# Kernel optimization log

Measured on AMD Instinct MI355X. Metric: run time of the kernel, lower is better.

## Reference

```python
import jax, jax.numpy as jnp
import numpy as np

N_HEAD = 16
LN_EPS = 1e-5


def setup_inputs() -> dict:
    key = jax.random.key(0)
    ks = jax.random.split(key, 12)
    B, S, D = 4, 1024, 1024
    s = 1.0 / np.sqrt(D)
    return {
        "Q": jax.random.normal(ks[0], (B, S, D), jnp.float32),
        "K": jax.random.normal(ks[1], (B, S, D), jnp.float32),
        "V": jax.random.normal(ks[2], (B, S, D), jnp.float32),
        # Linear weights stored torch-style [out, in]
        "Wq": jax.random.normal(ks[3], (D, D), jnp.float32) * s,
        "bq": jnp.zeros((D,), jnp.float32),
        "Wk": jax.random.normal(ks[4], (D, D), jnp.float32) * s,
        "bk": jnp.zeros((D,), jnp.float32),
        "Wv": jax.random.normal(ks[5], (D, D), jnp.float32) * s,
        "bv": jnp.zeros((D,), jnp.float32),
        "Wo": jax.random.normal(ks[6], (D, D), jnp.float32) * s,
        "bo": jnp.zeros((D,), jnp.float32),
        "ln_g": jnp.ones((D,), jnp.float32),
        "ln_b": jnp.zeros((D,), jnp.float32),
    }


def _layer_norm(x, g, b):
    mu = jnp.mean(x, axis=-1, keepdims=True)
    var = jnp.mean(jnp.square(x - mu), axis=-1, keepdims=True)
    return (x - mu) * jax.lax.rsqrt(var + LN_EPS) * g + b


def reference(Q, K, V, Wq, bq, Wk, bk, Wv, bv, Wo, bo, ln_g, ln_b):
    B, S, D = Q.shape
    H = N_HEAD
    dk = D // H
    # projections, split heads: [B, H, S, dk]
    q = (Q @ Wq.T + bq).reshape(B, S, H, dk).transpose(0, 2, 1, 3)
    k = (K @ Wk.T + bk).reshape(B, S, H, dk).transpose(0, 2, 1, 3)
    v = (V @ Wv.T + bv).reshape(B, S, H, dk).transpose(0, 2, 1, 3)
    scores = jnp.einsum("bhqd,bhkd->bhqk", q, k) / np.sqrt(dk)
    # NOTE: original module applies softmax twice (F.softmax then nn.Softmax)
    attn = jax.nn.softmax(jax.nn.softmax(scores, axis=-1), axis=-1)
    ctx = jnp.einsum("bhqk,bhkd->bhqd", attn, v)  # [B, H, S, dk]
    ctx = ctx.transpose(0, 2, 1, 3).reshape(B, S, D)
    out = ctx @ Wo.T + bo
    return _layer_norm(out + Q, ln_g, ln_b)
```

## Files before the change

### kernel.cpp

```cpp
#include <hip/hip_runtime.h>
#include <cstdint>
#include <cstddef>


typedef unsigned short ushort_t;
typedef __attribute__((ext_vector_type(8))) short bf16x8;
typedef __attribute__((ext_vector_type(8))) unsigned short us8;
typedef __attribute__((ext_vector_type(4))) unsigned short us4;
typedef __attribute__((ext_vector_type(4))) float f32x4;

#define MFMA16(a, b, c) __builtin_amdgcn_mfma_f32_16x16x32_bf16((a), (b), (c), 0, 0, 0)
#define EXP2F(x) __builtin_amdgcn_exp2f(x)
#define LOG2E 1.4426950408889634f

__device__ __forceinline__ float b2f(ushort_t u) {
  union { unsigned int i; float f; } x; x.i = ((unsigned int)u) << 16; return x.f;
}
__device__ __forceinline__ ushort_t f2b(float f) {
  union { unsigned int i; float f; } x; x.f = f;
  unsigned int r = (x.i + 0x7FFFu + ((x.i >> 16) & 1u)) >> 16;
  return (ushort_t)r;
}
__device__ __forceinline__ unsigned int cvtpk(float lo, float hi) {
  unsigned int r;
  asm("v_cvt_pk_bf16_f32 %0, %1, %2" : "=v"(r) : "v"(lo), "v"(hi));
  return r;
}
__device__ __forceinline__ us8 cvt8pk(float4 a, float4 b) {
  union { unsigned int u[4]; us8 v; } r;
  r.u[0] = cvtpk(a.x, a.y); r.u[1] = cvtpk(a.z, a.w);
  r.u[2] = cvtpk(b.x, b.y); r.u[3] = cvtpk(b.z, b.w);
  return r.v;
}

__device__ __forceinline__ void gll16(const ushort_t* g, ushort_t* l) {
  __builtin_amdgcn_global_load_lds(
      (const __attribute__((address_space(1))) void*)g,
      (__attribute__((address_space(3))) void*)l, 16, 0, 0);
}

__global__ __launch_bounds__(256, 8) void cvt4_kernel(
    const float* __restrict__ w0, const float* __restrict__ w1,
    const float* __restrict__ w2, const float* __restrict__ w3,
    ushort_t* __restrict__ dst) {
  const int which = blockIdx.y;
  const float* src = (which == 0) ? w0 : (which == 1) ? w1 : (which == 2) ? w2 : w3;
  const int i = (blockIdx.x * 256 + threadIdx.x) * 8;
  const float4 a = *(const float4*)(src + i);
  const float4 b = *(const float4*)(src + i + 4);
  *(us8*)(dst + (size_t)which * 1048576 + i) = cvt8pk(a, b);
}

__global__ __launch_bounds__(256, 3) void qkv_proj_kernel(
    const float* __restrict__ Qin, const float* __restrict__ Kin,
    const float* __restrict__ Vin,
    const ushort_t* __restrict__ wq, const ushort_t* __restrict__ wk,
    const ushort_t* __restrict__ wv,
    const float* __restrict__ bq, const float* __restrict__ bk,
    const float* __restrict__ bv,
    ushort_t* __restrict__ qb, ushort_t* __restrict__ kb,
    ushort_t* __restrict__ vb) {
  __shared__ __align__(16) ushort_t Asl0[128 * 32];
  __shared__ __align__(16) ushort_t Asl1[128 * 32];
  __shared__ __align__(16) ushort_t Bsl0[128 * 32];
  __shared__ __align__(16) ushort_t Bsl1[128 * 32];
  const float* A; const ushort_t* W; const float* bias; float scale;
  if (blockIdx.z == 0)      { A = Qin; W = wq; bias = bq; scale = 0.125f * LOG2E; }
  else if (blockIdx.z == 1) { A = Kin; W = wk; bias = bk; scale = 1.0f; }
  else                      { A = Vin; W = wv; bias = bv; scale = 1.0f; }
  const int l = blockIdx.x;
  const int xcd = l & 7, ii = l >> 3;
  const int m0 = (xcd * 4 + (ii >> 3)) * 128;
  const int n0 = (ii & 7) * 128;
  const int tid = threadIdx.x;
  const int wave = tid >> 6, lane = tid & 63;
  const int l15 = lane & 15, quad = lane >> 4;
  const int wr = wave >> 1, wc = wave & 1;

  const int ra = tid >> 2, ca = (tid & 3) * 8;
  const float* Ap0 = A + (size_t)(m0 + ra) * 1024 + ca;
  const float* Ap1 = A + (size_t)(m0 + ra + 64) * 1024 + ca;

  const ushort_t* Bg0 = W + (size_t)(n0 + wave * 32 + (lane >> 2)) * 1024 + (lane & 3) * 8;
  const ushort_t* Bg1 = W + (size_t)(n0 + wave * 32 + 16 + (lane >> 2)) * 1024 + (lane & 3) * 8;

  float4 xa0 = *(const float4*)(Ap0), xa1 = *(const float4*)(Ap0 + 4);
  float4 xa2 = *(const float4*)(Ap1), xa3 = *(const float4*)(Ap1 + 4);
  gll16(Bg0, Bsl0 + wave * 1024);
  gll16(Bg1, Bsl0 + wave * 1024 + 512);
  *(us8*)(Asl0 + ra * 32 + ca) = cvt8pk(xa0, xa1);
  *(us8*)(Asl0 + (ra + 64) * 32 + ca) = cvt8pk(xa2, xa3);
  float4 ya0 = *(const float4*)(Ap0 + 32), ya1 = *(const float4*)(Ap0 + 36);
  float4 ya2 = *(const float4*)(Ap1 + 32), ya3 = *(const float4*)(Ap1 + 36);
  asm volatile("s_waitcnt vmcnt(4) lgkmcnt(0)" ::: "memory");
  __builtin_amdgcn_s_barrier();

  f32x4 acc[4][4] = {};
#define QKV_COMPUTE(ASL, BSL)                                                   \
  {                                                                             \
    bf16x8 af[4], bfr[4];                                                       \
    _Pragma("unroll") for (int s = 0; s < 4; ++s)                               \
        af[s] = *(const bf16x8*)((ASL) + (wr * 64 + s * 16 + l15) * 32 + quad * 8); \
    _Pragma("unroll") for (int s = 0; s < 4; ++s)                               \
        bfr[s] = *(const bf16x8*)((BSL) + (wc * 64 + s * 16 + l15) * 32 + quad * 8); \
    _Pragma("unroll") for (int ms = 0; ms < 4; ++ms)                            \
        _Pragma("unroll") for (int ns = 0; ns < 4; ++ns)                        \
            acc[ms][ns] = MFMA16(af[ms], bfr[ns], acc[ms][ns]);                 \
  }

  for (int k0 = 0; k0 < 1024; k0 += 64) {
    {
      gll16(Bg0 + k0 + 32, Bsl1 + wave * 1024);
      gll16(Bg1 + k0 + 32, Bsl1 + wave * 1024 + 512);
      *(us8*)(Asl1 + ra * 32 + ca) = cvt8pk(ya0, ya1);
      *(us8*)(Asl1 + (ra + 64) * 32 + ca) = cvt8pk(ya2, ya3);
    }
    if (k0 + 64 < 1024) {
      xa0 = *(const float4*)(Ap0 + k0 + 64); xa1 = *(const float4*)(Ap0 + k0 + 68);
      xa2 = *(const float4*)(Ap1 + k0 + 64); xa3 = *(const float4*)(Ap1 + k0 + 68);
    }
    QKV_COMPUTE(Asl0, Bsl0)
    if (k0 + 64 < 1024) asm volatile("s_waitcnt vmcnt(4) lgkmcnt(0)" ::: "memory");
    else                asm volatile("s_waitcnt vmcnt(0) lgkmcnt(0)" ::: "memory");
    __builtin_amdgcn_s_barrier();
    if (k0 + 64 < 1024) {
      gll16(Bg0 + k0 + 64, Bsl0 + wave * 1024);
      gll16(Bg1 + k0 + 64, Bsl0 + wave * 1024 + 512);
      *(us8*)(Asl0 + ra * 32 + ca) = cvt8pk(xa0, xa1);
      *(us8*)(Asl0 + (ra + 64) * 32 + ca) = cvt8pk(xa2, xa3);
      if (k0 + 96 < 1024) {
        ya0 = *(const float4*)(Ap0 + k0 + 96); ya1 = *(const float4*)(Ap0 + k0 + 100);
        ya2 = *(const float4*)(Ap1 + k0 + 96); ya3 = *(const float4*)(Ap1 + k0 + 100);
      }
    }
    QKV_COMPUTE(Asl1, Bsl1)
    if (k0 + 96 < 1024)      asm volatile("s_waitcnt vmcnt(4) lgkmcnt(0)" ::: "memory");
    else                     asm volatile("s_waitcnt vmcnt(0) lgkmcnt(0)" ::: "memory");
    __builtin_amdgcn_s_barrier();
  }
#undef QKV_COMPUTE

  if (blockIdx.z != 2) {
    ushort_t* outp = (blockIdx.z == 0) ? qb : kb;
#pragma unroll
    for (int ns = 0; ns < 4; ++ns) {
      const int col = n0 + wc * 64 + ns * 16 + l15;
      const float bv_ = bias[col];
#pragma unroll
      for (int ms = 0; ms < 4; ++ms) {
        const int rowb = m0 + wr * 64 + ms * 16 + quad * 4;
#pragma unroll
        for (int r = 0; r < 4; ++r) {
          outp[(size_t)(rowb + r) * 1024 + col] =
              f2b((acc[ms][ns][r] + bv_) * scale);
        }
      }
    }
  } else {
#pragma unroll
    for (int ns = 0; ns < 4; ++ns) {
      const int col = n0 + wc * 64 + ns * 16 + l15;
      const float bv_ = bias[col];
      const int h = col >> 6, d = col & 63;
#pragma unroll
      for (int ms = 0; ms < 4; ++ms) {
        const int i0 = m0 + wr * 64 + ms * 16 + quad * 4;
        const int b = i0 >> 10, s0 = i0 & 1023;
        us4 pack;
#pragma unroll
        for (int r = 0; r < 4; ++r) pack[r] = f2b(acc[ms][ns][r] + bv_);
        *(us4*)(vb + ((size_t)(b * 16 + h) * 64 + d) * 1024 + s0) = pack;
      }
    }
  }
}

__global__ __launch_bounds__(256, 4) void attn_kernel(
    const ushort_t* __restrict__ qb, const ushort_t* __restrict__ kb,
    const ushort_t* __restrict__ vb, ushort_t* __restrict__ ctx) {
  __shared__ __align__(16) ushort_t Sh0[64 * 72];
  __shared__ __align__(16) ushort_t Sh1[64 * 72];
  __shared__ __align__(16) ushort_t Sh2[64 * 72];
  __shared__ __align__(16) ushort_t Sh3[64 * 72];

  const int tid = threadIdx.x, wave = tid >> 6, lane = tid & 63;
  const int l15 = lane & 15, quad = lane >> 4;
  const int l = blockIdx.x;
  const int xcd = l & 7, ii = l >> 3;
  const int bh = xcd * 8 + (ii >> 4);
  const int q0 = (ii & 15) * 64;
  const int b = bh >> 4, h = bh & 15;
  const ushort_t* qg = qb + ((size_t)b << 20) + h * 64;
  const ushort_t* kg = kb + ((size_t)b << 20) + h * 64;
  const ushort_t* vg = vb + ((size_t)bh << 16);

  const int kr0 = tid >> 3, kc0 = (tid & 7) * 8;
  const int kr1 = (tid + 256) >> 3, kc1 = kc0;
  const int o0 = kr0 * 72 + kc0, o1 = kr1 * 72 + kc1;

  *(us8*)(Sh0 + o0) = *(const us8*)(qg + (size_t)(q0 + kr0) * 1024 + kc0);
  *(us8*)(Sh0 + o1) = *(const us8*)(qg + (size_t)(q0 + kr1) * 1024 + kc1);
  us8 rk0 = *(const us8*)(kg + (size_t)kr0 * 1024 + kc0);
  us8 rk1 = *(const us8*)(kg + (size_t)kr1 * 1024 + kc1);
  *(us8*)(Sh1 + o0) = rk0;
  *(us8*)(Sh1 + o1) = rk1;
  rk0 = *(const us8*)(kg + (size_t)(64 + kr0) * 1024 + kc0);
  rk1 = *(const us8*)(kg + (size_t)(64 + kr1) * 1024 + kc1);
  __syncthreads();
  bf16x8 aqh[2];
  aqh[0] = *(const bf16x8*)(Sh0 + (wave * 16 + l15) * 72 + quad * 8);
  aqh[1] = *(const bf16x8*)(Sh0 + (wave * 16 + l15) * 72 + 32 + quad * 8);

  float z1 = 0.f;
  for (int kt = 0; kt < 16; ++kt) {
    const ushort_t* kcur = (kt & 1) ? Sh2 : Sh1;
    f32x4 sc[4] = {};
#pragma unroll
    for (int kk = 0; kk < 2; ++kk) {
#pragma unroll
      for (int ns = 0; ns < 4; ++ns) {
        const bf16x8 kf = *(const bf16x8*)(kcur + (ns * 16 + l15) * 72 + kk * 32 + quad * 8);
        sc[ns] = MFMA16(kf, aqh[kk], sc[ns]);
      }
    }
    if (kt < 15) {
      ushort_t* knxt = (kt & 1) ? Sh1 : Sh2;
      *(us8*)(knxt + o0) = rk0;
      *(us8*)(knxt + o1) = rk1;
      if (kt < 14) {
        rk0 = *(const us8*)(kg + (size_t)((kt + 2) * 64 + kr0) * 1024 + kc0);
        rk1 = *(const us8*)(kg + (size_t)((kt + 2) * 64 + kr1) * 1024 + kc1);
      }
    }
#pragma unroll
    for (int ns = 0; ns < 4; ++ns)
#pragma unroll
      for (int r = 0; r < 4; ++r) z1 += EXP2F(sc[ns][r]);
    asm volatile("s_waitcnt lgkmcnt(0)" ::: "memory");
    __builtin_amdgcn_s_barrier();
  }
  z1 += __shfl_xor(z1, 16, 64);
  z1 += __shfl_xor(z1, 32, 64);
  const float iz1 = LOG2E / z1;

  const int adr0 = ((((quad & 1) << 1) * 16) + l15) << 2;
  const int adr1 = adr0 + 64;

  f32x4 oac[4] = {};
  float z2 = 0.f;
  rk0 = *(const us8*)(kg + (size_t)kr0 * 1024 + kc0);
  rk1 = *(const us8*)(kg + (size_t)kr1 * 1024 + kc1);
  us8 rv0 = *(const us8*)(vg + (size_t)kr0 * 1024 + kc0);
  us8 rv1 = *(const us8*)(vg + (size_t)kr1 * 1024 + kc1);
  *(us8*)(Sh0 + o0) = rk0;
  *(us8*)(Sh0 + o1) = rk1;
  *(us8*)(Sh2 + o0) = rv0;
  *(us8*)(Sh2 + o1) = rv1;
  rk0 = *(const us8*)(kg + (size_t)(64 + kr0) * 1024 + kc0);
  rk1 = *(const us8*)(kg + (size_t)(64 + kr1) * 1024 + kc1);
  rv0 = *(const us8*)(vg + (size_t)kr0 * 1024 + 64 + kc0);
  rv1 = *(const us8*)(vg + (size_t)kr1 * 1024 + 64 + kc1);
  asm volatile("s_waitcnt lgkmcnt(0)" ::: "memory");
  __builtin_amdgcn_s_barrier();

  for (int kt = 0; kt < 16; ++kt) {
    const ushort_t* kcur = (kt & 1) ? Sh1 : Sh0;
    const ushort_t* vcur = (kt & 1) ? Sh3 : Sh2;
    f32x4 sc[4] = {};
#pragma unroll
    for (int kk = 0; kk < 2; ++kk) {
#pragma unroll
      for (int ns = 0; ns < 4; ++ns) {
        const bf16x8 kf = *(const bf16x8*)(kcur + (ns * 16 + l15) * 72 + kk * 32 + quad * 8);
        sc[ns] = MFMA16(kf, aqh[kk], sc[ns]);
      }
    }
    if (kt < 15) {
      ushort_t* knxt = (kt & 1) ? Sh0 : Sh1;
      ushort_t* vnxt = (kt & 1) ? Sh2 : Sh3;
      *(us8*)(knxt + o0) = rk0;
      *(us8*)(knxt + o1) = rk1;
      *(us8*)(vnxt + o0) = rv0;
      *(us8*)(vnxt + o1) = rv1;
      if (kt < 14) {
        rk0 = *(const us8*)(kg + (size_t)((kt + 2) * 64 + kr0) * 1024 + kc0);
        rk1 = *(const us8*)(kg + (size_t)((kt + 2) * 64 + kr1) * 1024 + kc1);
        rv0 = *(const us8*)(vg + (size_t)kr0 * 1024 + (kt + 2) * 64 + kc0);
        rv1 = *(const us8*)(vg + (size_t)kr1 * 1024 + (kt + 2) * 64 + kc1);
      }
    }
    unsigned int D[4][2];
#pragma unroll
    for (int ns = 0; ns < 4; ++ns) {
      const float e0 = EXP2F(EXP2F(sc[ns][0]) * iz1);
      const float e1 = EXP2F(EXP2F(sc[ns][1]) * iz1);
      const float e2 = EXP2F(EXP2F(sc[ns][2]) * iz1);
      const float e3 = EXP2F(EXP2F(sc[ns][3]) * iz1);
      z2 += (e0 + e1) + (e2 + e3);
      D[ns][0] = cvtpk(e0, e1);
      D[ns][1] = cvtpk(e2, e3);
    }
#pragma unroll
    for (int kk = 0; kk < 2; ++kk) {
      union { unsigned int u[4]; bf16x8 v; } pf;
#pragma unroll
      for (int t = 0; t < 4; ++t) {
        const int adr = (t >> 1) ? adr1 : adr0;
        const int lo = __builtin_amdgcn_ds_bpermute(adr, (int)D[2 * kk][t & 1]);
        const int hi = __builtin_amdgcn_ds_bpermute(adr, (int)D[2 * kk + 1][t & 1]);
        pf.u[t] = (unsigned int)((quad >= 2) ? hi : lo);
      }
#pragma unroll
      for (int ns2 = 0; ns2 < 4; ++ns2) {
        const bf16x8 vf = *(const bf16x8*)(vcur + (ns2 * 16 + l15) * 72 + kk * 32 + quad * 8);
        oac[ns2] = MFMA16(vf, pf.v, oac[ns2]);
      }
    }
    asm volatile("s_waitcnt lgkmcnt(0)" ::: "memory");
    __builtin_amdgcn_s_barrier();
  }

  z2 += __shfl_xor(z2, 16, 64);
  z2 += __shfl_xor(z2, 32, 64);
  const int s = q0 + wave * 16 + l15;
  ushort_t* crow = ctx + ((size_t)(b * 1024 + s)) * 1024 + h * 64;
#pragma unroll
  for (int ns2 = 0; ns2 < 4; ++ns2) {
    us4 pack;
#pragma unroll
    for (int r = 0; r < 4; ++r) pack[r] = f2b(oac[ns2][r] / z2);
    *(us4*)(crow + ns2 * 16 + quad * 4) = pack;
  }
}

__global__ __launch_bounds__(256, 4) void out_proj_kernel(
    const ushort_t* __restrict__ ctxp, const ushort_t* __restrict__ wo,
    const float* __restrict__ bo, ushort_t* __restrict__ pre) {
  __shared__ __align__(16) ushort_t Asl0[64 * 32];
  __shared__ __align__(16) ushort_t Asl1[64 * 32];
  __shared__ __align__(16) ushort_t Bsl0[128 * 32];
  __shared__ __align__(16) ushort_t Bsl1[128 * 32];
  const int tid = threadIdx.x;
  const int wave = tid >> 6, lane = tid & 63;
  const int l15 = lane & 15, quad = lane >> 4;
  const int wr = wave >> 1, wc = wave & 1;
  const int l = blockIdx.x;
  const int xcd = l & 7, ii = l >> 3;
  const int m0 = (xcd * 8 + (ii >> 3)) * 64;
  const int n0 = (ii & 7) * 128;

  const ushort_t* Ag = ctxp + (size_t)(m0 + wave * 16 + (lane >> 2)) * 1024 + (lane & 3) * 8;
  const ushort_t* Bg0 = wo + (size_t)(n0 + wave * 32 + (lane >> 2)) * 1024 + (lane & 3) * 8;
  const ushort_t* Bg1 = wo + (size_t)(n0 + wave * 32 + 16 + (lane >> 2)) * 1024 + (lane & 3) * 8;

  gll16(Ag, Asl0 + wave * 512);
  gll16(Bg0, Bsl0 + wave * 1024);
  gll16(Bg1, Bsl0 + wave * 1024 + 512);
  __syncthreads();

  f32x4 acc[2][4] = {};
#define OUTP_COMPUTE(ASL, BSL)                                                  \
  {                                                                             \
    bf16x8 af[2], bfr[4];                                                       \
    _Pragma("unroll") for (int s = 0; s < 2; ++s)                               \
        af[s] = *(const bf16x8*)((ASL) + (wr * 32 + s * 16 + l15) * 32 + quad * 8); \
    _Pragma("unroll") for (int s = 0; s < 4; ++s)                               \
        bfr[s] = *(const bf16x8*)((BSL) + (wc * 64 + s * 16 + l15) * 32 + quad * 8); \
    _Pragma("unroll") for (int ms = 0; ms < 2; ++ms)                            \
        _Pragma("unroll") for (int ns = 0; ns < 4; ++ns)                        \
            acc[ms][ns] = MFMA16(af[ms], bfr[ns], acc[ms][ns]);                 \
  }

  for (int k0 = 0; k0 < 1024; k0 += 64) {
    {
      gll16(Ag + k0 + 32, Asl1 + wave * 512);
      gll16(Bg0 + k0 + 32, Bsl1 + wave * 1024);
      gll16(Bg1 + k0 + 32, Bsl1 + wave * 1024 + 512);
    }
    OUTP_COMPUTE(Asl0, Bsl0)
    __syncthreads();
    if (k0 + 64 < 1024) {
      gll16(Ag + k0 + 64, Asl0 + wave * 512);
      gll16(Bg0 + k0 + 64, Bsl0 + wave * 1024);
      gll16(Bg1 + k0 + 64, Bsl0 + wave * 1024 + 512);
    }
    OUTP_COMPUTE(Asl1, Bsl1)
    __syncthreads();
  }
#undef OUTP_COMPUTE

#pragma unroll
  for (int ns = 0; ns < 4; ++ns) {
    const int col = n0 + wc * 64 + ns * 16 + l15;
    const float bv_ = bo[col];
#pragma unroll
    for (int ms = 0; ms < 2; ++ms) {
      const int rowb = m0 + wr * 32 + ms * 16 + quad * 4;
#pragma unroll
      for (int r = 0; r < 4; ++r) {
        pre[(size_t)(rowb + r) * 1024 + col] = f2b(acc[ms][ns][r] + bv_);
      }
    }
  }
}

__global__ __launch_bounds__(256, 4) void ln_kernel(
    const ushort_t* __restrict__ pre, const float* __restrict__ Q,
    const float* __restrict__ g, const float* __restrict__ bta,
    float* __restrict__ out) {
  const int row = blockIdx.x;
  const int tid = threadIdx.x;
  const size_t base = (size_t)row * 1024 + tid * 4;
  const ushort4 p4 = *(const ushort4*)(pre + base);
  const float4 q4 = *(const float4*)(Q + base);
  float v[4] = {b2f(p4.x) + q4.x, b2f(p4.y) + q4.y,
                b2f(p4.z) + q4.z, b2f(p4.w) + q4.w};
  float s1 = v[0] + v[1] + v[2] + v[3];
  float s2 = v[0]*v[0] + v[1]*v[1] + v[2]*v[2] + v[3]*v[3];
#pragma unroll
  for (int off = 1; off < 64; off <<= 1) {
    s1 += __shfl_xor(s1, off, 64);
    s2 += __shfl_xor(s2, off, 64);
  }
  __shared__ float r1[4], r2[4];
  const int wave = tid >> 6, lane = tid & 63;
  if (lane == 0) { r1[wave] = s1; r2[wave] = s2; }
  __syncthreads();
  const float t1 = r1[0] + r1[1] + r1[2] + r1[3];
  const float t2 = r2[0] + r2[1] + r2[2] + r2[3];
  const float mu = t1 * (1.0f / 1024.0f);
  const float var = t2 * (1.0f / 1024.0f) - mu * mu;
  const float inv = rsqrtf(var + 1e-5f);
  const int c0 = tid * 4;
#pragma unroll
  for (int j = 0; j < 4; ++j) {
    const int c = c0 + j;
    out[(size_t)row * 1024 + c] = (v[j] - mu) * inv * g[c] + bta[c];
  }
}

extern "C" void kernel_launch(void* const* d_in, const int* in_sizes, int n_in,
                              void* d_out, int out_size, void* d_ws, size_t ws_size,
                              hipStream_t stream) {
  const float* Q  = (const float*)d_in[0];
  const float* K  = (const float*)d_in[1];
  const float* V  = (const float*)d_in[2];
  const float* Wq = (const float*)d_in[3];
  const float* bq = (const float*)d_in[4];
  const float* Wk = (const float*)d_in[5];
  const float* bk = (const float*)d_in[6];
  const float* Wv = (const float*)d_in[7];
  const float* bv = (const float*)d_in[8];
  const float* Wo = (const float*)d_in[9];
  const float* bo = (const float*)d_in[10];
  const float* lg = (const float*)d_in[11];
  const float* lb = (const float*)d_in[12];

  char* ws = (char*)d_ws;
  ushort_t* qb  = (ushort_t*)(ws);
  ushort_t* kb  = (ushort_t*)(ws + ((size_t)8  << 20));
  ushort_t* vb  = (ushort_t*)(ws + ((size_t)16 << 20));
  ushort_t* pre = (ushort_t*)(ws);

  ushort_t* dptr  = (ushort_t*)d_out;
  ushort_t* wo_bf = dptr;
  ushort_t* wq_bf = dptr + 1048576;
  ushort_t* wk_bf = dptr + 2097152;
  ushort_t* wv_bf = dptr + 3145728;
  ushort_t* ctx   = dptr + 4194304;
  float*    out   = (float*)d_out;

  cvt4_kernel<<<dim3(512, 4), 256, 0, stream>>>(Wo, Wq, Wk, Wv, dptr);
  qkv_proj_kernel<<<dim3(256, 1, 3), 256, 0, stream>>>(Q, K, V, wq_bf, wk_bf, wv_bf,
                                                       bq, bk, bv, qb, kb, vb);
  attn_kernel<<<dim3(1024), 256, 0, stream>>>(qb, kb, vb, ctx);
  out_proj_kernel<<<dim3(512), 256, 0, stream>>>(ctx, wo_bf, bo, pre);
  ln_kernel<<<dim3(4096), 256, 0, stream>>>(pre, Q, lg, lb, out);
}
```

Before: 235.4 us.

## Triple-buffer weight tiles in QKV and output projection GEMMs

Both projection GEMMs move from double-buffered to triple-buffered LDS for the async global-to-LDS weight (and ctx) loads. Each load is now issued two k-steps ahead, and the waitcnt counts are relaxed so each barrier waits only for the oldest tile. The aim is to hide more global memory latency behind the MFMA work. In exchange it uses more LDS per block, which may reduce occupancy, and it adds pointer rotation plus peeled epilogue steps.

```diff
diff --git a/kernel.cpp b/kernel.cpp
--- a/kernel.cpp
+++ b/kernel.cpp
@@ -62,8 +62,7 @@
     ushort_t* __restrict__ vb) {
   __shared__ __align__(16) ushort_t Asl0[128 * 32];
   __shared__ __align__(16) ushort_t Asl1[128 * 32];
-  __shared__ __align__(16) ushort_t Bsl0[128 * 32];
-  __shared__ __align__(16) ushort_t Bsl1[128 * 32];
+  __shared__ __align__(16) ushort_t Bsl[3][128 * 32];
   const float* A; const ushort_t* W; const float* bias; float scale;
   if (blockIdx.z == 0)      { A = Qin; W = wq; bias = bq; scale = 0.125f * LOG2E; }
   else if (blockIdx.z == 1) { A = Kin; W = wk; bias = bk; scale = 1.0f; }
@@ -83,16 +82,21 @@
 
   const ushort_t* Bg0 = W + (size_t)(n0 + wave * 32 + (lane >> 2)) * 1024 + (lane & 3) * 8;
   const ushort_t* Bg1 = W + (size_t)(n0 + wave * 32 + 16 + (lane >> 2)) * 1024 + (lane & 3) * 8;
+  ushort_t* Ba = Bsl[0];
+  ushort_t* Bb = Bsl[1];
+  ushort_t* Bc = Bsl[2];
 
   float4 xa0 = *(const float4*)(Ap0), xa1 = *(const float4*)(Ap0 + 4);
   float4 xa2 = *(const float4*)(Ap1), xa3 = *(const float4*)(Ap1 + 4);
-  gll16(Bg0, Bsl0 + wave * 1024);
-  gll16(Bg1, Bsl0 + wave * 1024 + 512);
+  gll16(Bg0, Ba + wave * 1024);
+  gll16(Bg1, Ba + wave * 1024 + 512);
+  gll16(Bg0 + 32, Bb + wave * 1024);
+  gll16(Bg1 + 32, Bb + wave * 1024 + 512);
+  float4 ya0 = *(const float4*)(Ap0 + 32), ya1 = *(const float4*)(Ap0 + 36);
+  float4 ya2 = *(const float4*)(Ap1 + 32), ya3 = *(const float4*)(Ap1 + 36);
   *(us8*)(Asl0 + ra * 32 + ca) = cvt8pk(xa0, xa1);
   *(us8*)(Asl0 + (ra + 64) * 32 + ca) = cvt8pk(xa2, xa3);
-  float4 ya0 = *(const float4*)(Ap0 + 32), ya1 = *(const float4*)(Ap0 + 36);
-  float4 ya2 = *(const float4*)(Ap1 + 32), ya3 = *(const float4*)(Ap1 + 36);
-  asm volatile("s_waitcnt vmcnt(4) lgkmcnt(0)" ::: "memory");
+  asm volatile("s_waitcnt vmcnt(6) lgkmcnt(0)" ::: "memory");
   __builtin_amdgcn_s_barrier();
 
   f32x4 acc[4][4] = {};
@@ -108,36 +112,34 @@
             acc[ms][ns] = MFMA16(af[ms], bfr[ns], acc[ms][ns]);                 \
   }
 
-  for (int k0 = 0; k0 < 1024; k0 += 64) {
-    {
-      gll16(Bg0 + k0 + 32, Bsl1 + wave * 1024);
-      gll16(Bg1 + k0 + 32, Bsl1 + wave * 1024 + 512);
-      *(us8*)(Asl1 + ra * 32 + ca) = cvt8pk(ya0, ya1);
-      *(us8*)(Asl1 + (ra + 64) * 32 + ca) = cvt8pk(ya2, ya3);
-    }
-    if (k0 + 64 < 1024) {
-      xa0 = *(const float4*)(Ap0 + k0 + 64); xa1 = *(const float4*)(Ap0 + k0 + 68);
-      xa2 = *(const float4*)(Ap1 + k0 + 64); xa3 = *(const float4*)(Ap1 + k0 + 68);
-    }
-    QKV_COMPUTE(Asl0, Bsl0)
-    if (k0 + 64 < 1024) asm volatile("s_waitcnt vmcnt(4) lgkmcnt(0)" ::: "memory");
-    else                asm volatile("s_waitcnt vmcnt(0) lgkmcnt(0)" ::: "memory");
+  for (int i = 0; i < 15; ++i) {
+    const int k0 = i * 64;
+    gll16(Bg0 + k0 + 64, Bc + wave * 1024);
+    gll16(Bg1 + k0 + 64, Bc + wave * 1024 + 512);
+    xa0 = *(const float4*)(Ap0 + k0 + 64); xa1 = *(const float4*)(Ap0 + k0 + 68);
+    xa2 = *(const float4*)(Ap1 + k0 + 64); xa3 = *(const float4*)(Ap1 + k0 + 68);
+    QKV_COMPUTE(Asl0, Ba)
+    *(us8*)(Asl1 + ra * 32 + ca) = cvt8pk(ya0, ya1);
+    *(us8*)(Asl1 + (ra + 64) * 32 + ca) = cvt8pk(ya2, ya3);
+    asm volatile("s_waitcnt vmcnt(6) lgkmcnt(0)" ::: "memory");
     __builtin_amdgcn_s_barrier();
-    if (k0 + 64 < 1024) {
-      gll16(Bg0 + k0 + 64, Bsl0 + wave * 1024);
-      gll16(Bg1 + k0 + 64, Bsl0 + wave * 1024 + 512);
-      *(us8*)(Asl0 + ra * 32 + ca) = cvt8pk(xa0, xa1);
-      *(us8*)(Asl0 + (ra + 64) * 32 + ca) = cvt8pk(xa2, xa3);
-      if (k0 + 96 < 1024) {
-        ya0 = *(const float4*)(Ap0 + k0 + 96); ya1 = *(const float4*)(Ap0 + k0 + 100);
-        ya2 = *(const float4*)(Ap1 + k0 + 96); ya3 = *(const float4*)(Ap1 + k0 + 100);
-      }
-    }
-    QKV_COMPUTE(Asl1, Bsl1)
-    if (k0 + 96 < 1024)      asm volatile("s_waitcnt vmcnt(4) lgkmcnt(0)" ::: "memory");
-    else                     asm volatile("s_waitcnt vmcnt(0) lgkmcnt(0)" ::: "memory");
+    gll16(Bg0 + k0 + 96, Ba + wave * 1024);
+    gll16(Bg1 + k0 + 96, Ba + wave * 1024 + 512);
+    ya0 = *(const float4*)(Ap0 + k0 + 96); ya1 = *(const float4*)(Ap0 + k0 + 100);
+    ya2 = *(const float4*)(Ap1 + k0 + 96); ya3 = *(const float4*)(Ap1 + k0 + 100);
+    QKV_COMPUTE(Asl1, Bb)
+    *(us8*)(Asl0 + ra * 32 + ca) = cvt8pk(xa0, xa1);
+    *(us8*)(Asl0 + (ra + 64) * 32 + ca) = cvt8pk(xa2, xa3);
+    asm volatile("s_waitcnt vmcnt(6) lgkmcnt(0)" ::: "memory");
     __builtin_amdgcn_s_barrier();
-  }
+    ushort_t* t = Ba; Ba = Bc; Bc = Bb; Bb = t;
+  }
+  QKV_COMPUTE(Asl0, Ba)
+  *(us8*)(Asl1 + ra * 32 + ca) = cvt8pk(ya0, ya1);
+  *(us8*)(Asl1 + (ra + 64) * 32 + ca) = cvt8pk(ya2, ya3);
+  asm volatile("s_waitcnt vmcnt(0) lgkmcnt(0)" ::: "memory");
+  __builtin_amdgcn_s_barrier();
+  QKV_COMPUTE(Asl1, Bb)
 #undef QKV_COMPUTE
 
   if (blockIdx.z != 2) {
@@ -336,10 +338,8 @@
 __global__ __launch_bounds__(256, 4) void out_proj_kernel(
     const ushort_t* __restrict__ ctxp, const ushort_t* __restrict__ wo,
     const float* __restrict__ bo, ushort_t* __restrict__ pre) {
-  __shared__ __align__(16) ushort_t Asl0[64 * 32];
-  __shared__ __align__(16) ushort_t Asl1[64 * 32];
-  __shared__ __align__(16) ushort_t Bsl0[128 * 32];
-  __shared__ __align__(16) ushort_t Bsl1[128 * 32];
+  __shared__ __align__(16) ushort_t Abuf[3][64 * 32];
+  __shared__ __align__(16) ushort_t Bbuf[3][128 * 32];
   const int tid = threadIdx.x;
   const int wave = tid >> 6, lane = tid & 63;
   const int l15 = lane & 15, quad = lane >> 4;
@@ -353,10 +353,17 @@
   const ushort_t* Bg0 = wo + (size_t)(n0 + wave * 32 + (lane >> 2)) * 1024 + (lane & 3) * 8;
   const ushort_t* Bg1 = wo + (size_t)(n0 + wave * 32 + 16 + (lane >> 2)) * 1024 + (lane & 3) * 8;
 
-  gll16(Ag, Asl0 + wave * 512);
-  gll16(Bg0, Bsl0 + wave * 1024);
-  gll16(Bg1, Bsl0 + wave * 1024 + 512);
-  __syncthreads();
+  ushort_t* Aa = Abuf[0]; ushort_t* Ab = Abuf[1]; ushort_t* Ac = Abuf[2];
+  ushort_t* Ba = Bbuf[0]; ushort_t* Bb = Bbuf[1]; ushort_t* Bc = Bbuf[2];
+
+  gll16(Ag, Aa + wave * 512);
+  gll16(Bg0, Ba + wave * 1024);
+  gll16(Bg1, Ba + wave * 1024 + 512);
+  gll16(Ag + 32, Ab + wave * 512);
+  gll16(Bg0 + 32, Bb + wave * 1024);
+  gll16(Bg1 + 32, Bb + wave * 1024 + 512);
+  asm volatile("s_waitcnt vmcnt(3)" ::: "memory");
+  __builtin_amdgcn_s_barrier();
 
   f32x4 acc[2][4] = {};
 #define OUTP_COMPUTE(ASL, BSL)                                                  \
@@ -371,22 +378,21 @@
             acc[ms][ns] = MFMA16(af[ms], bfr[ns], acc[ms][ns]);                 \
   }
 
-  for (int k0 = 0; k0 < 1024; k0 += 64) {
-    {
-      gll16(Ag + k0 + 32, Asl1 + wave * 512);
-      gll16(Bg0 + k0 + 32, Bsl1 + wave * 1024);
-      gll16(Bg1 + k0 + 32, Bsl1 + wave * 1024 + 512);
-    }
-    OUTP_COMPUTE(Asl0, Bsl0)
-    __syncthreads();
-    if (k0 + 64 < 1024) {
-      gll16(Ag + k0 + 64, Asl0 + wave * 512);
-      gll16(Bg0 + k0 + 64, Bsl0 + wave * 1024);
-      gll16(Bg1 + k0 + 64, Bsl0 + wave * 1024 + 512);
-    }
-    OUTP_COMPUTE(Asl1, Bsl1)
-    __syncthreads();
-  }
+  for (int p = 0; p < 30; ++p) {
+    const int k = p * 32;
+    gll16(Ag + k + 64, Ac + wave * 512);
+    gll16(Bg0 + k + 64, Bc + wave * 1024);
+    gll16(Bg1 + k + 64, Bc + wave * 1024 + 512);
+    OUTP_COMPUTE(Aa, Ba)
+    asm volatile("s_waitcnt vmcnt(3) lgkmcnt(0)" ::: "memory");
+    __builtin_amdgcn_s_barrier();
+    ushort_t* ta = Aa; Aa = Ab; Ab = Ac; Ac = ta;
+    ushort_t* tb = Ba; Ba = Bb; Bb = Bc; Bc = tb;
+  }
+  OUTP_COMPUTE(Aa, Ba)
+  asm volatile("s_waitcnt vmcnt(0) lgkmcnt(0)" ::: "memory");
+  __builtin_amdgcn_s_barrier();
+  OUTP_COMPUTE(Ab, Bb)
 #undef OUTP_COMPUTE
 
 #pragma unroll
```

Result: no change. 237.9 us (+1.0%).
